# Kernel tuning notes

Measured on AMD Instinct MI355X. Metric: run time of the kernel, lower is better.

The kernel has to match this reference:

```python
import jax, jax.numpy as jnp
import numpy as np

# Module hyperparameters (match init_kwargs)
T0, Z0, T1, Z1, K, S, ROUTING = 4, 16, 8, 16, 5, 1, 3
PAD = 2  # hard-coded padding=2 in the torch module
N, H, W_SP = 4, 128, 128


def setup_inputs() -> dict:
    key = jax.random.key(0)
    k1, k2 = jax.random.split(key)
    u = jax.random.normal(k1, (N, T0, Z0, H, W_SP), dtype=jnp.float32)
    # t_0 independent Conv2d(z_0 -> t_1*z_1, k, s, padding=2, bias=False) weights
    W = jax.random.normal(k2, (T0, T1 * Z1, Z0, K, K), dtype=jnp.float32) * 0.05
    return {"u": u, "W": W}


def _squash(p):
    # squash along last (z_1) axis, matching torch: p_norm = sqrt(|p|^2 + 1e-9)
    n2 = jnp.sum(p * p, axis=-1, keepdims=True)
    n = jnp.sqrt(n2 + 1e-9)
    return n2 / (1.0 + n2) * p / n


def _capsule_convs(u, W):
    # t_0 independent convs == one grouped conv with feature_group_count=t_0
    n, t0, z0, h, w = u.shape
    x = u.reshape(n, t0 * z0, h, w)
    wk = W.reshape(t0 * T1 * Z1, z0, K, K)
    y = jax.lax.conv_general_dilated(
        x, wk, window_strides=(S, S), padding=[(PAD, PAD), (PAD, PAD)],
        dimension_numbers=("NCHW", "OIHW", "NCHW"), feature_group_count=t0)
    h1, w1 = y.shape[2], y.shape[3]
    # [N, t0*t1*z1, H1, W1] -> u_hat [t0, N, H1, W1, t1, z1]
    y = y.reshape(n, t0, T1, Z1, h1, w1)
    return jnp.transpose(y, (1, 0, 4, 5, 2, 3))


def _routing(u_hat):
    t0, n, h, w, t1, z1 = u_hat.shape
    dt = u_hat.dtype
    b = jnp.zeros((t0, n, t1, h, w), dt)  # NCHW layout per capsule type
    neg_inf = jnp.array(-jnp.inf, dt)
    zero = jnp.array(0.0, dt)
    win = (1, 1, 1, K, K)
    ones = (1, 1, 1, 1, 1)
    pad = [(0, 0), (0, 0), (0, 0), (PAD, PAD), (PAD, PAD)]
    v = None
    for d in range(ROUTING):
        uh = jax.lax.stop_gradient(u_hat) if d < ROUTING - 1 else u_hat
        # stability max: max_pool2d(k,1,pad=2) (pads with -inf) then max over t1
        b_max = jax.lax.reduce_window(b, neg_inf, jax.lax.max, win, ones, pad)
        b_max = jnp.max(b_max, axis=2, keepdims=True)
        c = jnp.exp(b - b_max)  # [t0, N, t1, H, W]
        # conv2d_same with ones kernel [1,t1,k,k] == channel-sum then kxk box-sum
        sum_c = jax.lax.reduce_window(jnp.sum(c, axis=2, keepdims=True), zero,
                                      jax.lax.add, win, ones, pad)
        r = c / sum_c                                   # [t0, N, t1, H, W]
        r = jnp.transpose(r, (0, 1, 3, 4, 2))[..., None]  # [t0,N,H,W,t1,1]
        p = jnp.sum(r * uh, axis=0)                     # [N, H, W, t1, z1]
        v = _squash(p)
        # NOTE: the original torch code computes b + (u_hat*v).sum(4) into a
        # list `b_t_list_` that is never assigned back, so b stays zero across
        # iterations. We faithfully reproduce that (no b update).
    return jnp.transpose(v, (0, 3, 4, 1, 2))  # [N, t1, z1, H, W]


def reference(u, W):
    return _routing(_capsule_convs(u, W))
```

## Files before the change

### kernel.cpp

```cpp
#include <hip/hip_runtime.h>
#include <hip/hip_bf16.h>


#define CO 128

typedef __attribute__((ext_vector_type(8))) short bf16x8;
typedef __attribute__((ext_vector_type(4))) float f32x4;

__global__ __launch_bounds__(256) void k_pre(const float* __restrict__ u,
                                             const float* __restrict__ Wsrc,
                                             ushort* __restrict__ ut,
                                             ushort* __restrict__ Wr2) {
    int b = blockIdx.x;
    int t = threadIdx.x;
    if (b >= 1024) {
        int base = (b - 1024) * 2048 + t;
#pragma unroll
        for (int j = 0; j < 8; ++j) {
            int idx = base + j * 256;
            int ci = idx & 63;
            int r  = idx >> 6;
            int co = r & 127;
            int kk = r >> 7;
            int t0 = ci >> 4, z0 = ci & 15;
            __hip_bfloat16 bb = __float2bfloat16(Wsrc[((t0 * CO + co) * 16 + z0) * 25 + kk]);
            Wr2[idx] = *(ushort*)&bb;
        }
        return;
    }
    __shared__ float lt[64][65];
    int wc = b & 1; int nh = b >> 1; int h = nh & 127; int n = nh >> 7;
    int w0 = wc * 64;
    int w = t & 63; int cg = t >> 6;
    const float* up = u + (size_t)n * (64 * 128 * 128) + h * 128 + w0 + w;
#pragma unroll
    for (int i = 0; i < 16; ++i) {
        int ci = cg * 16 + i;
        lt[w][ci] = up[(size_t)ci * (128 * 128)];
    }
    __syncthreads();
    int ci2 = t & 63; int pg = t >> 6;
    ushort* op = ut + (((size_t)(n * 128 + h)) * 128 + w0) * 64 + ci2;
#pragma unroll
    for (int i = 0; i < 16; ++i) {
        int w2 = pg * 16 + i;
        __hip_bfloat16 bv = __float2bfloat16(lt[w2][ci2]);
        op[(size_t)w2 * 64] = *(ushort*)&bv;
    }
}

__global__ __launch_bounds__(256, 2) void k_caps(const ushort* __restrict__ ut,
                                                 const ushort* __restrict__ Wr2,
                                                 float* __restrict__ out) {
    __shared__ ushort As[240 * 80];

    int tid = threadIdx.x;
    int bid = blockIdx.x;
    int bx = bid & 7, by = (bid >> 3) & 15, n = bid >> 7;
    int h0 = by * 8, w0 = bx * 16;

    int lane = tid & 63, wid = tid >> 6;
    int wm4  = (wid >> 1) * 4;
    int wn64 = (wid & 1) * 64;
    int q = lane >> 4, m16 = lane & 15;

    const ushort* bpb = Wr2 + (wn64 + m16) * 64 + q * 8;

    bf16x8 bn1[4], bn2[4];
#pragma unroll
    for (int ni = 0; ni < 4; ++ni) {
        bn1[ni] = *(const bf16x8*)(bpb + ni * 1024);
        bn2[ni] = *(const bf16x8*)(bpb + 5 * 8192 + ni * 1024);
    }

    for (int i = tid; i < 1920; i += 256) {
        int p = i >> 3, c = i & 7;
        int rr = p / 20, cc = p - rr * 20;
        int hh = h0 + rr - 2, ww = w0 + cc - 2;
        bf16x8 v = {};
        if ((unsigned)hh < 128u && (unsigned)ww < 128u)
            v = *(const bf16x8*)(ut + (((size_t)(n * 128 + hh)) * 128 + ww) * 64 + c * 8);
        *(bf16x8*)&As[p * 80 + c * 8] = v;
    }
    __syncthreads();

    f32x4 acc[4][4] = {};
    int aBase = (wm4 * 20 + m16) * 80 + q * 8;

#pragma unroll
    for (int kw = 0; kw < 5; ++kw) {
#pragma unroll
        for (int ks = 0; ks < 2; ++ks) {
            bf16x8 a[8];
#pragma unroll
            for (int r = 0; r < 8; ++r)
                a[r] = *(const bf16x8*)&As[aBase + (r * 20 + kw) * 80 + ks * 32];
#pragma unroll
            for (int kh = 0; kh < 5; ++kh) {
                const int s = kw * 10 + ks * 5 + kh;
                bf16x8 bc[4];
#pragma unroll
                for (int ni = 0; ni < 4; ++ni) { bc[ni] = bn1[ni]; bn1[ni] = bn2[ni]; }
                const int s2 = s + 2;
                if (s2 < 50) {
                    const int kw2 = s2 / 10, ks2 = (s2 / 5) & 1, kh2 = s2 % 5;
                    const int off2 = (kh2 * 5 + kw2) * 8192 + ks2 * 32;
#pragma unroll
                    for (int ni = 0; ni < 4; ++ni)
                        bn2[ni] = *(const bf16x8*)(bpb + off2 + ni * 1024);
                }
#pragma unroll
                for (int mi = 0; mi < 4; ++mi)
#pragma unroll
                    for (int ni = 0; ni < 4; ++ni)
                        acc[mi][ni] = __builtin_amdgcn_mfma_f32_16x16x32_bf16(
                            a[mi + kh], bc[ni], acc[mi][ni], 0, 0, 0);
            }
        }
    }

#pragma unroll
    for (int mi = 0; mi < 4; ++mi) {
        int h = h0 + wm4 + mi;
        int hlo = h - 2; if (hlo < 0) hlo = 0;
        int hhi = h + 2; if (hhi > 127) hhi = 127;
        float cnth = (float)(hhi - hlo + 1);
#pragma unroll
        for (int ni = 0; ni < 4; ++ni) {
            f32x4 cv = acc[mi][ni];
            float ov[4];
#pragma unroll
            for (int reg = 0; reg < 4; ++reg) {
                int w = w0 + q * 4 + reg;
                int wlo = w - 2; if (wlo < 0) wlo = 0;
                int whi = w + 2; if (whi > 127) whi = 127;
                float s = 1.f / (8.f * cnth * (float)(whi - wlo + 1));
                float pv = cv[reg] * s;
                float n2 = pv * pv;
                n2 += __shfl_xor(n2, 1);
                n2 += __shfl_xor(n2, 2);
                n2 += __shfl_xor(n2, 4);
                n2 += __shfl_xor(n2, 8);
                float fac = n2 / ((1.f + n2) * sqrtf(n2 + 1e-9f));
                ov[reg] = pv * fac;
            }
            int co = wn64 + ni * 16 + m16;
            *(float4*)(out + (((size_t)(n * CO + co)) << 14) + h * 128 + w0 + q * 4) =
                make_float4(ov[0], ov[1], ov[2], ov[3]);
        }
    }
}

extern "C" void kernel_launch(void* const* d_in, const int* in_sizes, int n_in,
                              void* d_out, int out_size, void* d_ws, size_t ws_size,
                              hipStream_t stream) {
    const float* u    = (const float*)d_in[0];
    const float* Wsrc = (const float*)d_in[1];
    float* out = (float*)d_out;
    ushort* Wr2 = (ushort*)d_ws;
    ushort* ut  = (ushort*)((char*)d_ws + 409600);

    k_pre<<<1124, 256, 0, stream>>>(u, Wsrc, ut, Wr2);
    k_caps<<<512, 256, 0, stream>>>(ut, Wr2, out);
}
```

Baseline: 133.2 us.

## Stage conv weights through shared memory with register prefetch per phase

Reorders the bf16 weight layout in the prep kernel into phase-contiguous (kw,ks) chunks. The conv kernel now loads each phase's weights cooperatively and coalesced into a padded LDS buffer, prefetching the next phase into registers, instead of each wave loading its B fragments directly from global memory. This is meant to cut redundant global/L2 traffic and latency. In exchange it adds two barriers per phase and about 43KB of extra LDS, which may reduce occupancy below two blocks per CU.

```diff
diff --git a/kernel.cpp b/kernel.cpp
--- a/kernel.cpp
+++ b/kernel.cpp
@@ -10,7 +10,7 @@
 __global__ __launch_bounds__(256) void k_pre(const float* __restrict__ u,
                                              const float* __restrict__ Wsrc,
                                              ushort* __restrict__ ut,
-                                             ushort* __restrict__ Wr2) {
+                                             ushort* __restrict__ Wr3) {
     int b = blockIdx.x;
     int t = threadIdx.x;
     if (b >= 1024) {
@@ -18,13 +18,18 @@
 #pragma unroll
         for (int j = 0; j < 8; ++j) {
             int idx = base + j * 256;
-            int ci = idx & 63;
-            int r  = idx >> 6;
-            int co = r & 127;
-            int kk = r >> 7;
+            int ci_l = idx & 31;
+            int r    = idx >> 5;
+            int co   = r & 127;
+            int r2   = r >> 7;
+            int kh   = r2 % 5;
+            int kwks = r2 / 5;
+            int ks = kwks & 1, kw = kwks >> 1;
+            int ci = ks * 32 + ci_l;
             int t0 = ci >> 4, z0 = ci & 15;
+            int kk = kh * 5 + kw;
             __hip_bfloat16 bb = __float2bfloat16(Wsrc[((t0 * CO + co) * 16 + z0) * 25 + kk]);
-            Wr2[idx] = *(ushort*)&bb;
+            Wr3[idx] = *(ushort*)&bb;
         }
         return;
     }
@@ -50,9 +55,10 @@
 }
 
 __global__ __launch_bounds__(256, 2) void k_caps(const ushort* __restrict__ ut,
-                                                 const ushort* __restrict__ Wr2,
+                                                 const ushort* __restrict__ Wr3,
                                                  float* __restrict__ out) {
     __shared__ ushort As[240 * 80];
+    __shared__ ushort Bs[5 * 128 * 34];
 
     int tid = threadIdx.x;
     int bid = blockIdx.x;
@@ -64,15 +70,6 @@
     int wn64 = (wid & 1) * 64;
     int q = lane >> 4, m16 = lane & 15;
 
-    const ushort* bpb = Wr2 + (wn64 + m16) * 64 + q * 8;
-
-    bf16x8 bn1[4], bn2[4];
-#pragma unroll
-    for (int ni = 0; ni < 4; ++ni) {
-        bn1[ni] = *(const bf16x8*)(bpb + ni * 1024);
-        bn2[ni] = *(const bf16x8*)(bpb + 5 * 8192 + ni * 1024);
-    }
-
     for (int i = tid; i < 1920; i += 256) {
         int p = i >> 3, c = i & 7;
         int rr = p / 20, cc = p - rr * 20;
@@ -82,39 +79,51 @@
             v = *(const bf16x8*)(ut + (((size_t)(n * 128 + hh)) * 128 + ww) * 64 + c * 8);
         *(bf16x8*)&As[p * 80 + c * 8] = v;
     }
-    __syncthreads();
+
+    bf16x8 pre[10];
+#pragma unroll
+    for (int j = 0; j < 10; ++j)
+        pre[j] = *(const bf16x8*)(Wr3 + (size_t)(tid + j * 256) * 8);
 
     f32x4 acc[4][4] = {};
     int aBase = (wm4 * 20 + m16) * 80 + q * 8;
+    int bBase = (wn64 + m16) * 34 + q * 8;
 
 #pragma unroll
     for (int kw = 0; kw < 5; ++kw) {
 #pragma unroll
         for (int ks = 0; ks < 2; ++ks) {
+            const int ph = kw * 2 + ks;
+            __syncthreads();
+#pragma unroll
+            for (int j = 0; j < 10; ++j) {
+                int c = tid + j * 256;
+                int kh_ = c >> 9, rem = c & 511;
+                *(bf16x8*)&Bs[(kh_ * 128 + (rem >> 2)) * 34 + (rem & 3) * 8] = pre[j];
+            }
+            __syncthreads();
+            if (ph < 9) {
+                const ushort* src = Wr3 + (size_t)(ph + 1) * 20480;
+#pragma unroll
+                for (int j = 0; j < 10; ++j)
+                    pre[j] = *(const bf16x8*)(src + (size_t)(tid + j * 256) * 8);
+            }
             bf16x8 a[8];
 #pragma unroll
             for (int r = 0; r < 8; ++r)
                 a[r] = *(const bf16x8*)&As[aBase + (r * 20 + kw) * 80 + ks * 32];
 #pragma unroll
             for (int kh = 0; kh < 5; ++kh) {
-                const int s = kw * 10 + ks * 5 + kh;
-                bf16x8 bc[4];
+                bf16x8 bb[4];
 #pragma unroll
-                for (int ni = 0; ni < 4; ++ni) { bc[ni] = bn1[ni]; bn1[ni] = bn2[ni]; }
-                const int s2 = s + 2;
-                if (s2 < 50) {
-                    const int kw2 = s2 / 10, ks2 = (s2 / 5) & 1, kh2 = s2 % 5;
-                    const int off2 = (kh2 * 5 + kw2) * 8192 + ks2 * 32;
-#pragma unroll
-                    for (int ni = 0; ni < 4; ++ni)
-                        bn2[ni] = *(const bf16x8*)(bpb + off2 + ni * 1024);
-                }
+                for (int ni = 0; ni < 4; ++ni)
+                    bb[ni] = *(const bf16x8*)&Bs[kh * (128 * 34) + bBase + ni * (16 * 34)];
 #pragma unroll
                 for (int mi = 0; mi < 4; ++mi)
 #pragma unroll
                     for (int ni = 0; ni < 4; ++ni)
                         acc[mi][ni] = __builtin_amdgcn_mfma_f32_16x16x32_bf16(
-                            a[mi + kh], bc[ni], acc[mi][ni], 0, 0, 0);
+                            a[mi + kh], bb[ni], acc[mi][ni], 0, 0, 0);
             }
         }
     }
@@ -157,9 +166,9 @@
     const float* u    = (const float*)d_in[0];
     const float* Wsrc = (const float*)d_in[1];
     float* out = (float*)d_out;
-    ushort* Wr2 = (ushort*)d_ws;
+    ushort* Wr3 = (ushort*)d_ws;
     ushort* ut  = (ushort*)((char*)d_ws + 409600);
 
-    k_pre<<<1124, 256, 0, stream>>>(u, Wsrc, ut, Wr2);
-    k_caps<<<512, 256, 0, stream>>>(ut, Wr2, out);
+    k_pre<<<1124, 256, 0, stream>>>(u, Wsrc, ut, Wr3);
+    k_caps<<<512, 256, 0, stream>>>(ut, Wr3, out);
 }
```

New measurement: 111.8 us. 16.1% less time.
